# Kernel tuning notes

Measured on AMD Instinct MI355X. Metric: run time of the kernel, lower is better.

The kernel has to match this reference:

```python
import jax, jax.numpy as jnp
import numpy as np

H = 8; DH = 32; MAX_HOP = 256; NUM_EDGE = 25
NHOP = MAX_HOP + 2   # 258 (incl. UNREACHABLE)
NEDGE = NUM_EDGE + 2 # 27  (incl. NO_EDGE)


def _ln(x, g, b, eps=1e-5):
    m = x.mean(-1, keepdims=True)
    v = ((x - m) ** 2).mean(-1, keepdims=True)
    return (x - m) / jnp.sqrt(v + eps) * g + b


def _scatter_bins(att, idx, M):
    # att: [B,H,N,N] probs, idx: [B,N,N] int bins -> [B,H,N,M] scatter-add over keys
    B, Hh, N, _ = att.shape
    idxb = jnp.broadcast_to(idx[:, None, :, :], att.shape)
    bi = jnp.arange(B)[:, None, None, None]
    hi = jnp.arange(Hh)[None, :, None, None]
    ni = jnp.arange(N)[None, None, :, None]
    return jnp.zeros((B, Hh, N, M), att.dtype).at[bi, hi, ni, idxb].add(att)


def _forward(x, mask, distance_mat, edge_attr_mat,
             node_W, node_b, ln1_g, ln1_b, Wq, bq, Wk, bk, Wv, bv, Wo, bo,
             ln2_g, ln2_b, W1, b1, W2, b2,
             q_hop, q_edge, k_hop, k_edge, v_hop, v_edge,
             fln_g, fln_b, out_W, out_b):
    B, N, _ = x.shape
    h = x @ node_W + node_b  # [B,N,DM]
    # index preprocessing (clamp then -1 -> sentinel, as in torch)
    dist = jnp.minimum(distance_mat, MAX_HOP)
    dist = jnp.where(dist == -1, MAX_HOP + 1, dist)
    edge = jnp.minimum(edge_attr_mat, NUM_EDGE)
    edge = jnp.where(edge == -1, NUM_EDGE + 1, edge)

    # ---- encoder layer ----
    y = _ln(h, ln1_g, ln1_b)
    q = (y @ Wq + bq).reshape(B, N, H, DH).transpose(0, 2, 1, 3)  # bhnd
    k = (y @ Wk + bk).reshape(B, N, H, DH).transpose(0, 2, 1, 3)
    v = (y @ Wv + bv).reshape(B, N, H, DH).transpose(0, 2, 1, 3)
    Qh = q_hop.reshape(NHOP, H, DH).transpose(1, 0, 2)   # [H,M,d]
    Qe = q_edge.reshape(NEDGE, H, DH).transpose(1, 0, 2)
    Kh = k_hop.reshape(NHOP, H, DH).transpose(1, 0, 2)
    Ke = k_edge.reshape(NEDGE, H, DH).transpose(1, 0, 2)
    Vh = v_hop.reshape(NHOP, H, DH).transpose(1, 0, 2)
    Ve = v_edge.reshape(NEDGE, H, DH).transpose(1, 0, 2)

    dist_b = jnp.broadcast_to(dist[:, None, :, :], (B, H, N, N))
    edge_b = jnp.broadcast_to(edge[:, None, :, :], (B, H, N, N))

    qh = jnp.einsum('bhnd,hmd->bhnm', q, Qh)  # [B,H,N,M]
    query_hop = jnp.take_along_axis(qh, dist_b, axis=3)
    qe = jnp.einsum('bhnd,hmd->bhnm', q, Qe)
    query_edge = jnp.take_along_axis(qe, edge_b, axis=3)
    kh = jnp.einsum('bhnd,hmd->bhnm', k, Kh)
    # torch gathers along dim 2 of kh^T: key_hop[b,h,i,j] = k_j . Kh[dist[i,j]]
    key_hop = jnp.take_along_axis(jnp.swapaxes(kh, 2, 3), dist_b, axis=2)
    ke = jnp.einsum('bhnd,hmd->bhnm', k, Ke)
    key_edge = jnp.take_along_axis(ke, edge_b, axis=3)

    scale = DH ** (-0.5)
    scores = (jnp.einsum('bhid,bhjd->bhij', q, k)
              + (query_hop + key_hop) + (query_edge + key_edge)) * scale
    scores = jnp.where(mask[:, None, None, :], -jnp.inf, scores)
    att = jax.nn.softmax(scores, axis=-1)

    vha = _scatter_bins(att, dist, NHOP)   # [B,H,N,NHOP]
    vea = _scatter_bins(att, edge, NEDGE)
    ctx = (jnp.einsum('bhij,bhjd->bhid', att, v)
           + jnp.einsum('bhim,hmd->bhid', vha, Vh)
           + jnp.einsum('bhim,hmd->bhid', vea, Ve))
    ctx = ctx.transpose(0, 2, 1, 3).reshape(B, N, H * DH)
    h = h + (ctx @ Wo + bo)

    y = _ln(h, ln2_g, ln2_b)
    y = jax.nn.gelu(y @ W1 + b1, approximate=False) @ W2 + b2
    h = h + y
    # ---- head ----
    out = _ln(h, fln_g, fln_b)
    return out @ out_W + out_b


def setup_inputs() -> dict:
    key = jax.random.key(0)
    ks = jax.random.split(key, 40)
    D_IN, DM, FF, OUT, B, N = 128, 256, 1024, 128, 16, 512
    nrm = lambda k, shape, s=0.02: jax.random.normal(k, shape, jnp.float32) * s
    z = lambda shape: jnp.zeros(shape, jnp.float32)
    o = lambda shape: jnp.ones(shape, jnp.float32)
    return {
        'x': jax.random.normal(ks[0], (B, N, D_IN), jnp.float32),
        'mask': jnp.zeros((B, N), bool),
        'distance_mat': jax.random.randint(ks[1], (B, N, N), 0, 257),
        'edge_attr_mat': jax.random.randint(ks[2], (B, N, N), 0, 26),
        'node_W': nrm(ks[3], (D_IN, DM)), 'node_b': z((DM,)),
        'ln1_g': o((DM,)), 'ln1_b': z((DM,)),
        'Wq': nrm(ks[4], (DM, DM)), 'bq': z((DM,)),
        'Wk': nrm(ks[5], (DM, DM)), 'bk': z((DM,)),
        'Wv': nrm(ks[6], (DM, DM)), 'bv': z((DM,)),
        'Wo': nrm(ks[7], (DM, DM)), 'bo': z((DM,)),
        'ln2_g': o((DM,)), 'ln2_b': z((DM,)),
        'W1': nrm(ks[8], (DM, FF)), 'b1': z((FF,)),
        'W2': nrm(ks[9], (FF, DM)), 'b2': z((DM,)),
        'q_hop': nrm(ks[10], (NHOP, DM)), 'q_edge': nrm(ks[11], (NEDGE, DM)),
        'k_hop': nrm(ks[12], (NHOP, DM)), 'k_edge': nrm(ks[13], (NEDGE, DM)),
        'v_hop': nrm(ks[14], (NHOP, DM)), 'v_edge': nrm(ks[15], (NEDGE, DM)),
        'fln_g': o((DM,)), 'fln_b': z((DM,)),
        'out_W': nrm(ks[16], (DM, OUT)), 'out_b': z((OUT,)),
    }


def reference(x, mask, distance_mat, edge_attr_mat,
              node_W, node_b, ln1_g, ln1_b, Wq, bq, Wk, bk, Wv, bv, Wo, bo,
              ln2_g, ln2_b, W1, b1, W2, b2,
              q_hop, q_edge, k_hop, k_edge, v_hop, v_edge,
              fln_g, fln_b, out_W, out_b):
    return _forward(x, mask, distance_mat, edge_attr_mat,
                    node_W, node_b, ln1_g, ln1_b, Wq, bq, Wk, bk, Wv, bv, Wo, bo,
                    ln2_g, ln2_b, W1, b1, W2, b2,
                    q_hop, q_edge, k_hop, k_edge, v_hop, v_edge,
                    fln_g, fln_b, out_W, out_b)
```

## Files before the change

kernel.cpp:

```cpp
#include <hip/hip_runtime.h>
#include <hip/hip_bf16.h>
#include <math.h>

#define BB 16
#define NN 512
#define DIN 128
#define DM 256
#define NH 8
#define DH 32
#define FF 1024
#define DOUT 128
#define NHOP 258
#define NEDGE 27
#define ROWS (BB*NN)
#define QHE_S 296

typedef short short8 __attribute__((ext_vector_type(8)));
typedef float f32x4 __attribute__((ext_vector_type(4)));

static __device__ __forceinline__ float bf2f(unsigned short u) {
    union { float f; unsigned int i; } c; c.i = ((unsigned int)u) << 16; return c.f;
}
static __device__ __forceinline__ short f2bs(float f) {
    __hip_bfloat16 h = __float2bfloat16(f);
    return *reinterpret_cast<short*>(&h);
}

__global__ __launch_bounds__(256) void k_ln(const float* __restrict__ in, const float* __restrict__ g,
                                            const float* __restrict__ bta, float* __restrict__ out) {
    int row = blockIdx.x * 4 + (threadIdx.x >> 6);
    int l = threadIdx.x & 63;
    float4 xv = ((const float4*)(in + (size_t)row*DM))[l];
    float s = xv.x + xv.y + xv.z + xv.w;
    #pragma unroll
    for (int o = 32; o > 0; o >>= 1) s += __shfl_xor(s, o, 64);
    float mean = s * (1.0f/DM);
    float dx = xv.x-mean, dy = xv.y-mean, dz = xv.z-mean, dw = xv.w-mean;
    float vs = dx*dx + dy*dy + dz*dz + dw*dw;
    #pragma unroll
    for (int o = 32; o > 0; o >>= 1) vs += __shfl_xor(vs, o, 64);
    float r = rsqrtf(vs * (1.0f/DM) + 1e-5f);
    float4 gg = ((const float4*)g)[l];
    float4 bb = ((const float4*)bta)[l];
    float4 ov; ov.x = dx*r*gg.x+bb.x; ov.y = dy*r*gg.y+bb.y; ov.z = dz*r*gg.z+bb.z; ov.w = dw*r*gg.w+bb.w;
    ((float4*)(out + (size_t)row*DM))[l] = ov;
}

template<int K, int N, int ACT, int RES, int QKV>
__global__ __launch_bounds__(256) void k_mgemm(const float* __restrict__ A, const float* __restrict__ W,
                                               const float* __restrict__ bias, float* __restrict__ out) {
    __shared__ __align__(16) short As[64][40];
    __shared__ __align__(16) short Bs[64][40];
    int r0 = blockIdx.x * 64;
    int n0 = blockIdx.y * 64;
    int tid = threadIdx.x;
    int w = tid >> 6, l = tid & 63;

    f32x4 acc[4];
    #pragma unroll
    for (int c = 0; c < 4; ++c) acc[c] = (f32x4){0.f,0.f,0.f,0.f};

    for (int k0 = 0; k0 < K; k0 += 32) {
        __syncthreads();
        {
            int m = tid >> 2, ks = (tid & 3) * 8;
            const float* src = A + (size_t)(r0 + m)*K + k0 + ks;
            float4 f0 = *(const float4*)src;
            float4 f1 = *(const float4*)(src + 4);
            short8 pk;
            pk[0]=f2bs(f0.x); pk[1]=f2bs(f0.y); pk[2]=f2bs(f0.z); pk[3]=f2bs(f0.w);
            pk[4]=f2bs(f1.x); pk[5]=f2bs(f1.y); pk[6]=f2bs(f1.z); pk[7]=f2bs(f1.w);
            *(short8*)&As[m][ks] = pk;
        }
        {
            int n = tid & 63, kg = tid >> 6;
            const float* wp = W + (size_t)(k0 + kg*8)*N + n0 + n;
            short8 pk;
            #pragma unroll
            for (int j = 0; j < 8; ++j) pk[j] = f2bs(wp[(size_t)j*N]);
            *(short8*)&Bs[n][kg*8] = pk;
        }
        __syncthreads();
        short8 af = *(short8*)&As[w*16 + (l & 15)][(l >> 4)*8];
        #pragma unroll
        for (int c = 0; c < 4; ++c) {
            short8 bf = *(short8*)&Bs[c*16 + (l & 15)][(l >> 4)*8];
            acc[c] = __builtin_amdgcn_mfma_f32_16x16x32_bf16(af, bf, acc[c], 0, 0, 0);
        }
    }

    int quad = l >> 4;
    #pragma unroll
    for (int c = 0; c < 4; ++c) {
        int col = n0 + c*16 + (l & 15);
        float bv = bias[col];
        #pragma unroll
        for (int reg = 0; reg < 4; ++reg) {
            int row = r0 + w*16 + quad*4 + reg;
            float val = acc[c][reg] + bv;
            if (ACT) val = 0.5f * val * (1.0f + erff(val * 0.70710678118654752f));
            if (QKV) {
                int b = row >> 9, n = row & (NN-1);
                int hh = col >> 5, d = col & (DH-1);
                out[(size_t)((b*NH + hh)*NN + n)*DH + d] = val;
            } else if (RES) {
                out[(size_t)row*N + col] += val;
            } else {
                out[(size_t)row*N + col] = val;
            }
        }
    }
}

__global__ __launch_bounds__(256) void k_prep(const float* __restrict__ q_hop, const float* __restrict__ q_edge,
                                              const float* __restrict__ k_edge, const float* __restrict__ v_hop,
                                              const float* __restrict__ v_edge,
                                              unsigned short* __restrict__ w2, unsigned short* __restrict__ vhve_d) {
    int h = blockIdx.x;
    int tid = threadIdx.x;
    for (int idx = tid; idx < 304*64; idx += 256) {
        int n = idx >> 6, kk = idx & 63;
        float val = 0.f;
        if (n < NHOP && kk < 32) val = q_hop[(size_t)n*DM + h*DH + kk];
        else if (n >= 264 && n < 264 + NEDGE) {
            int e = n - 264;
            val = (kk < 32) ? q_edge[(size_t)e*DM + h*DH + kk]
                            : k_edge[(size_t)e*DM + h*DH + (kk - 32)];
        }
        w2[((size_t)h*304 + n)*64 + kk] = (unsigned short)f2bs(val);
    }
    for (int idx = tid; idx < 32*320; idx += 256) {
        int d = idx / 320, kk = idx - d*320;
        float val = 0.f;
        if (kk < NHOP) val = v_hop[(size_t)kk*DM + h*DH + d];
        else if (kk >= 264 && kk < 264 + NEDGE) val = v_edge[(size_t)(kk-264)*DM + h*DH + d];
        vhve_d[((size_t)h*32 + d)*320 + kk] = (unsigned short)f2bs(val);
    }
}

__global__ __launch_bounds__(256) void k_tx(const float* __restrict__ k, float* __restrict__ kT) {
    __shared__ float lds[64*33];
    int bh = blockIdx.x;
    int j0 = blockIdx.y * 64;
    int tid = threadIdx.x;
    {
        int jj = tid >> 2, d8 = tid & 3;
        const float* src = k + ((size_t)bh*NN + j0 + jj)*DH + d8*8;
        float4 a = *(const float4*)(src);
        float4 b = *(const float4*)(src + 4);
        float* dst = lds + jj*33 + d8*8;
        dst[0]=a.x; dst[1]=a.y; dst[2]=a.z; dst[3]=a.w;
        dst[4]=b.x; dst[5]=b.y; dst[6]=b.z; dst[7]=b.w;
    }
    __syncthreads();
    {
        int d = tid >> 3, jg = tid & 7;
        float* dst = kT + ((size_t)bh*DH + d)*NN + j0;
        #pragma unroll
        for (int jj2 = 0; jj2 < 8; ++jj2) {
            int j = jg*8 + jj2;
            dst[j] = lds[j*33 + d];
        }
    }
}

__global__ __launch_bounds__(256) void k_kht2(const float* __restrict__ k, const float* __restrict__ k_hop,
                                              __hip_bfloat16* __restrict__ kht) {
    __shared__ __align__(16) short kb[512][40];
    int bh = blockIdx.x;
    int hh = bh & (NH-1);
    int r0 = blockIdx.y * 64;
    int tid = threadIdx.x;
    int w = tid >> 6, l = tid & 63;
    int quad = l >> 4, lr = l & 15;

    #pragma unroll
    for (int t = 0; t < 8; ++t) {
        int idx = tid + t*256;
        int row = idx >> 2, c = idx & 3;
        const float* src = k + ((size_t)bh*NN + row)*DH + c*8;
        float4 f0 = *(const float4*)src;
        float4 f1 = *(const float4*)(src + 4);
        short8 pk;
        pk[0]=f2bs(f0.x); pk[1]=f2bs(f0.y); pk[2]=f2bs(f0.z); pk[3]=f2bs(f0.w);
        pk[4]=f2bs(f1.x); pk[5]=f2bs(f1.y); pk[6]=f2bs(f1.z); pk[7]=f2bs(f1.w);
        *(short8*)&kb[row][c*8] = pk;
    }
    int m = r0 + w*16 + lr;
    int mc = m < NHOP ? m : NHOP-1;
    const float* ar = k_hop + (size_t)mc*DM + hh*DH + quad*8;
    float4 a0 = *(const float4*)ar;
    float4 a1 = *(const float4*)(ar + 4);
    short8 af;
    af[0]=f2bs(a0.x); af[1]=f2bs(a0.y); af[2]=f2bs(a0.z); af[3]=f2bs(a0.w);
    af[4]=f2bs(a1.x); af[5]=f2bs(a1.y); af[6]=f2bs(a1.z); af[7]=f2bs(a1.w);
    __syncthreads();

    for (int ct = 0; ct < 32; ++ct) {
        short8 bf = *(short8*)&kb[ct*16 + lr][quad*8];
        f32x4 acc = (f32x4){0.f,0.f,0.f,0.f};
        acc = __builtin_amdgcn_mfma_f32_16x16x32_bf16(af, bf, acc, 0, 0, 0);
        #pragma unroll
        for (int reg = 0; reg < 4; ++reg) {
            int m2 = r0 + w*16 + quad*4 + reg;
            if (m2 < NHOP)
                kht[((size_t)bh*NHOP + m2)*NN + ct*16 + lr] = __float2bfloat16(acc[reg]);
        }
    }
}

__global__ __launch_bounds__(256) void k_qhe2(const float* __restrict__ q, const float* __restrict__ k,
                                              const unsigned short* __restrict__ w2,
                                              unsigned short* __restrict__ qhe) {
    int bh = blockIdx.x;
    int hh = bh & (NH-1);
    int r0 = blockIdx.y * 64;
    int tid = threadIdx.x;
    int w = tid >> 6, l = tid & 63;
    int quad = l >> 4, lr = l & 15;

    const float* qr = q + ((size_t)bh*NN + r0 + w*16 + lr)*DH + quad*8;
    const float* kr = k + ((size_t)bh*NN + r0 + w*16 + lr)*DH + quad*8;
    float4 f0 = *(const float4*)qr, f1 = *(const float4*)(qr + 4);
    short8 af0;
    af0[0]=f2bs(f0.x); af0[1]=f2bs(f0.y); af0[2]=f2bs(f0.z); af0[3]=f2bs(f0.w);
    af0[4]=f2bs(f1.x); af0[5]=f2bs(f1.y); af0[6]=f2bs(f1.z); af0[7]=f2bs(f1.w);
    f0 = *(const float4*)kr; f1 = *(const float4*)(kr + 4);
    short8 af1;
    af1[0]=f2bs(f0.x); af1[1]=f2bs(f0.y); af1[2]=f2bs(f0.z); af1[3]=f2bs(f0.w);
    af1[4]=f2bs(f1.x); af1[5]=f2bs(f1.y); af1[6]=f2bs(f1.z); af1[7]=f2bs(f1.w);

    const unsigned short* w2h = w2 + (size_t)hh*304*64;
    for (int ct = 0; ct < 19; ++ct) {
        int col = ct*16 + lr;
        short8 b0 = *(const short8*)(w2h + (size_t)col*64 + quad*8);
        short8 b1 = *(const short8*)(w2h + (size_t)col*64 + 32 + quad*8);
        f32x4 acc = (f32x4){0.f,0.f,0.f,0.f};
        acc = __builtin_amdgcn_mfma_f32_16x16x32_bf16(af0, b0, acc, 0, 0, 0);
        acc = __builtin_amdgcn_mfma_f32_16x16x32_bf16(af1, b1, acc, 0, 0, 0);
        if (col < QHE_S) {
            #pragma unroll
            for (int reg = 0; reg < 4; ++reg) {
                int row = r0 + w*16 + quad*4 + reg;
                qhe[((size_t)bh*NN + row)*QHE_S + col] = (unsigned short)f2bs(acc[reg]);
            }
        }
    }
}

__global__ __launch_bounds__(256) void k_score(
    const float* __restrict__ q, const float* __restrict__ kT, const float* __restrict__ v,
    const __hip_bfloat16* __restrict__ kht, const int* __restrict__ dist, const int* __restrict__ edge,
    const unsigned char* __restrict__ mask, unsigned short* __restrict__ qhe,
    float* __restrict__ ctx)
{
    int g   = blockIdx.x;
    int r   = g >> 3;
    int b   = (g & 7) + ((r >> 8) << 3);
    int rem = r & 255;
    int i0  = (rem >> 1) * 4;
    int hg  = rem & 1;
    int w   = threadIdx.x >> 6;
    int l   = threadIdx.x & 63;
    int hh  = hg*4 + w;
    int bh  = b*NH + hh;

    __shared__ unsigned short mje[4][NN];
    __shared__ float qv[4][4][DH];
    __shared__ __hip_bfloat16 pb[4][4][NN];
    __shared__ float bins[4][292];

    {
        int t = threadIdx.x;
        int row = t >> 6, c0 = t & 63;
        #pragma unroll
        for (int rep = 0; rep < 2; ++rep) {
            int c4 = c0 + rep*64;
            int4 dv = ((const int4*)(dist + ((size_t)(b*NN) + i0 + row)*NN))[c4];
            int4 ev = ((const int4*)(edge + ((size_t)(b*NN) + i0 + row)*NN))[c4];
            int m0 = dv.x > 256 ? 256 : dv.x; if (dv.x < 0) m0 = 257;
            int m1 = dv.y > 256 ? 256 : dv.y; if (dv.y < 0) m1 = 257;
            int m2 = dv.z > 256 ? 256 : dv.z; if (dv.z < 0) m2 = 257;
            int m3 = dv.w > 256 ? 256 : dv.w; if (dv.w < 0) m3 = 257;
            int e0 = ev.x > 25 ? 25 : ev.x; if (ev.x < 0) e0 = 26;
            int e1 = ev.y > 25 ? 25 : ev.y; if (ev.y < 0) e1 = 26;
            int e2 = ev.z > 25 ? 25 : ev.z; if (ev.z < 0) e2 = 26;
            int e3 = ev.w > 25 ? 25 : ev.w; if (ev.w < 0) e3 = 26;
            mje[row][c4*4+0] = (unsigned short)(m0 | (e0 << 9));
            mje[row][c4*4+1] = (unsigned short)(m1 | (e1 << 9));
            mje[row][c4*4+2] = (unsigned short)(m2 | (e2 << 9));
            mje[row][c4*4+3] = (unsigned short)(m3 | (e3 << 9));
        }
        #pragma unroll
        for (int rep = 0; rep < 2; ++rep) {
            int i = rep*2 + (l >> 5), d = l & 31;
            qv[w][i][d] = q[((size_t)bh*NN + i0 + i)*DH + d];
        }
        for (int s = l; s < 292; s += 64) bins[w][s] = 0.f;
    }
    __syncthreads();

    float sc[4][8];
    #pragma unroll
    for (int i = 0; i < 4; ++i)
        #pragma unroll
        for (int s = 0; s < 8; ++s) sc[i][s] = 0.f;
    {
        const float* kTb = kT + (size_t)bh*DH*NN;
        for (int d = 0; d < 32; ++d) {
            const float* kr = kTb + (size_t)d*NN + l;
            float k0 = kr[0],   k1 = kr[64],  k2 = kr[128], k3 = kr[192];
            float k4 = kr[256], k5 = kr[320], k6 = kr[384], k7 = kr[448];
            float qa = qv[w][0][d], qb = qv[w][1][d], qc = qv[w][2][d], qd = qv[w][3][d];
            sc[0][0]+=qa*k0; sc[0][1]+=qa*k1; sc[0][2]+=qa*k2; sc[0][3]+=qa*k3;
            sc[0][4]+=qa*k4; sc[0][5]+=qa*k5; sc[0][6]+=qa*k6; sc[0][7]+=qa*k7;
            sc[1][0]+=qb*k0; sc[1][1]+=qb*k1; sc[1][2]+=qb*k2; sc[1][3]+=qb*k3;
            sc[1][4]+=qb*k4; sc[1][5]+=qb*k5; sc[1][6]+=qb*k6; sc[1][7]+=qb*k7;
            sc[2][0]+=qc*k0; sc[2][1]+=qc*k1; sc[2][2]+=qc*k2; sc[2][3]+=qc*k3;
            sc[2][4]+=qc*k4; sc[2][5]+=qc*k5; sc[2][6]+=qc*k6; sc[2][7]+=qc*k7;
            sc[3][0]+=qd*k0; sc[3][1]+=qd*k1; sc[3][2]+=qd*k2; sc[3][3]+=qd*k3;
            sc[3][4]+=qd*k4; sc[3][5]+=qd*k5; sc[3][6]+=qd*k6; sc[3][7]+=qd*k7;
        }
    }

    const __hip_bfloat16* khtb = kht + (size_t)bh*NHOP*NN;
    const unsigned char* mrow = mask + (size_t)b*NN;
    unsigned char msk[8];
    #pragma unroll
    for (int s = 0; s < 8; ++s) msk[s] = mrow[l + 64*s];
    const float scale = 0.17677669529663687f;

    #pragma unroll
    for (int i = 0; i < 4; ++i) {
        unsigned short* qhr = qhe + ((size_t)bh*NN + i0 + i)*QHE_S;
        int pk[8];
        #pragma unroll
        for (int s = 0; s < 8; ++s) pk[s] = mje[i][l + 64*s];
        unsigned short raw[8];
        #pragma unroll
        for (int s = 0; s < 8; ++s)
            raw[s] = ((const unsigned short*)khtb)[(size_t)(pk[s] & 511)*NN + l + 64*s];
        unsigned short qhv[8], qev[8];
        #pragma unroll
        for (int s = 0; s < 8; ++s) qhv[s] = qhr[pk[s] & 511];
        #pragma unroll
        for (int s = 0; s < 8; ++s) qev[s] = qhr[264 + (pk[s] >> 9)];
        float x[8];
        #pragma unroll
        for (int s = 0; s < 8; ++s) {
            float a = (sc[i][s] + bf2f(qhv[s]) + bf2f(raw[s]) + bf2f(qev[s])) * scale;
            if (msk[s]) a = -INFINITY;
            x[s] = a;
        }
        float mx = x[0];
        #pragma unroll
        for (int s = 1; s < 8; ++s) mx = fmaxf(mx, x[s]);
        #pragma unroll
        for (int o = 32; o > 0; o >>= 1) mx = fmaxf(mx, __shfl_xor(mx, o, 64));
        float sum = 0.f;
        #pragma unroll
        for (int s = 0; s < 8; ++s) { x[s] = __expf(x[s] - mx); sum += x[s]; }
        #pragma unroll
        for (int o = 32; o > 0; o >>= 1) sum += __shfl_xor(sum, o, 64);
        float inv = 1.0f / sum;
        #pragma unroll
        for (int s = 0; s < 8; ++s) {
            float ps = x[s] * inv;
            pb[w][i][l + 64*s] = __float2bfloat16(ps);
            atomicAdd(&bins[w][pk[s] & 511], ps);
            atomicAdd(&bins[w][264 + (pk[s] >> 9)], ps);
        }
        #pragma unroll
        for (int s5 = 0; s5 < 5; ++s5) {
            int idx = l + 64*s5;
            if (idx < 292) {
                qhr[idx] = (unsigned short)f2bs(bins[w][idx]);
                if (i < 3) bins[w][idx] = 0.f;
            }
        }
    }

    int jc = l >> 3, d4 = l & 7;
    float4 acc[4];
    #pragma unroll
    for (int i = 0; i < 4; ++i) { acc[i].x = acc[i].y = acc[i].z = acc[i].w = 0.f; }
    {
        const float* vb = v + (size_t)bh*NN*DH + d4*4;
        for (int off = 0; off < 64; ++off) {
            int j = 8*off + jc;
            float4 vv = *(const float4*)(vb + (size_t)j*DH);
            #pragma unroll
            for (int i = 0; i < 4; ++i) {
                float p = bf2f(*(const unsigned short*)&pb[w][i][j]);
                acc[i].x += p*vv.x; acc[i].y += p*vv.y; acc[i].z += p*vv.z; acc[i].w += p*vv.w;
            }
        }
    }
    #pragma unroll
    for (int i = 0; i < 4; ++i) {
        #pragma unroll
        for (int o = 8; o <= 32; o <<= 1) {
            acc[i].x += __shfl_xor(acc[i].x, o, 64);
            acc[i].y += __shfl_xor(acc[i].y, o, 64);
            acc[i].z += __shfl_xor(acc[i].z, o, 64);
            acc[i].w += __shfl_xor(acc[i].w, o, 64);
        }
        if (jc == 0) {
            *(float4*)(ctx + ((size_t)b*NN + i0 + i)*DM + hh*DH + d4*4) = acc[i];
        }
    }
}

__global__ __launch_bounds__(256) void k_av2(const unsigned short* __restrict__ vha,
                                             const unsigned short* __restrict__ vhve_d,
                                             float* __restrict__ ctx) {
    int bh = blockIdx.x;
    int hh = bh & (NH-1);
    int b  = bh >> 3;
    int r0 = blockIdx.y * 64;
    int tid = threadIdx.x;
    int w = tid >> 6, l = tid & 63;
    int quad = l >> 4, lr = l & 15;

    const unsigned short* arow = vha + ((size_t)bh*NN + r0 + w*16 + lr)*QHE_S + quad*8;
    const unsigned short* br0  = vhve_d + ((size_t)hh*32 + lr)*320 + quad*8;
    const unsigned short* br1  = vhve_d + ((size_t)hh*32 + 16 + lr)*320 + quad*8;

    f32x4 acc0 = (f32x4){0.f,0.f,0.f,0.f};
    f32x4 acc1 = (f32x4){0.f,0.f,0.f,0.f};
    #pragma unroll
    for (int k0 = 0; k0 < 320; k0 += 32) {
        short8 af = *(const short8*)(arow + k0);
        short8 b0 = *(const short8*)(br0 + k0);
        short8 b1 = *(const short8*)(br1 + k0);
        acc0 = __builtin_amdgcn_mfma_f32_16x16x32_bf16(af, b0, acc0, 0, 0, 0);
        acc1 = __builtin_amdgcn_mfma_f32_16x16x32_bf16(af, b1, acc1, 0, 0, 0);
    }
    #pragma unroll
    for (int reg = 0; reg < 4; ++reg) {
        int row = r0 + w*16 + quad*4 + reg;
        float* cp = ctx + ((size_t)b*NN + row)*DM + hh*DH;
        cp[lr]      += acc0[reg];
        cp[16 + lr] += acc1[reg];
    }
}

extern "C" void kernel_launch(void* const* d_in, const int* in_sizes, int n_in,
                              void* d_out, int out_size, void* d_ws, size_t ws_size,
                              hipStream_t stream) {
    const float* x     = (const float*)d_in[0];
    const unsigned char* mask = (const unsigned char*)d_in[1];
    const int*   dist  = (const int*)d_in[2];
    const int*   edge  = (const int*)d_in[3];
    const float* node_W = (const float*)d_in[4];
    const float* node_b = (const float*)d_in[5];
    const float* ln1_g = (const float*)d_in[6];
    const float* ln1_b = (const float*)d_in[7];
    const float* Wq = (const float*)d_in[8];
    const float* bq = (const float*)d_in[9];
    const float* Wk = (const float*)d_in[10];
    const float* bk = (const float*)d_in[11];
    const float* Wv = (const float*)d_in[12];
    const float* bv = (const float*)d_in[13];
    const float* Wo = (const float*)d_in[14];
    const float* bo = (const float*)d_in[15];
    const float* ln2_g = (const float*)d_in[16];
    const float* ln2_b = (const float*)d_in[17];
    const float* W1 = (const float*)d_in[18];
    const float* b1 = (const float*)d_in[19];
    const float* W2 = (const float*)d_in[20];
    const float* b2 = (const float*)d_in[21];
    const float* q_hop  = (const float*)d_in[22];
    const float* q_edge = (const float*)d_in[23];
    const float* k_hop  = (const float*)d_in[24];
    const float* k_edge = (const float*)d_in[25];
    const float* v_hop  = (const float*)d_in[26];
    const float* v_edge = (const float*)d_in[27];
    const float* fln_g = (const float*)d_in[28];
    const float* fln_b = (const float*)d_in[29];
    const float* out_W = (const float*)d_in[30];
    const float* out_b = (const float*)d_in[31];
    float* out = (float*)d_out;

    float* ws = (float*)d_ws;
    float* h   = ws + 0;
    float* y   = ws + 2097152;
    float* q   = ws + 4194304;
    float* k   = ws + 6291456;
    float* v   = ws + 8388608;
    float* ctx = ws + 10485760;
    __hip_bfloat16* kht = (__hip_bfloat16*)(ws + 12582912);
    float* ffn = ws + 12582912;
    float* kT  = ws + 21037056;
    unsigned short* qhe = (unsigned short*)(ws + 23134208);
    unsigned short* w2     = (unsigned short*)(y);
    unsigned short* vhve_d = (unsigned short*)(y + 81920);

    k_mgemm<DIN, DM, 0, 0, 0><<<dim3(ROWS/64, DM/64), 256, 0, stream>>>(x, node_W, node_b, h);
    k_ln<<<ROWS/4, 256, 0, stream>>>(h, ln1_g, ln1_b, y);
    k_mgemm<DM, DM, 0, 0, 1><<<dim3(ROWS/64, DM/64), 256, 0, stream>>>(y, Wq, bq, q);
    k_mgemm<DM, DM, 0, 0, 1><<<dim3(ROWS/64, DM/64), 256, 0, stream>>>(y, Wk, bk, k);
    k_mgemm<DM, DM, 0, 0, 1><<<dim3(ROWS/64, DM/64), 256, 0, stream>>>(y, Wv, bv, v);
    k_prep<<<NH, 256, 0, stream>>>(q_hop, q_edge, k_edge, v_hop, v_edge, w2, vhve_d);
    k_tx<<<dim3(BB*NH, 8), 256, 0, stream>>>(k, kT);
    k_kht2<<<dim3(BB*NH, 5), 256, 0, stream>>>(k, k_hop, kht);
    k_qhe2<<<dim3(BB*NH, NN/64), 256, 0, stream>>>(q, k, w2, qhe);
    k_score<<<BB*(NN/4)*2, 256, 0, stream>>>(q, kT, v, kht, dist, edge, mask, qhe, ctx);
    k_av2<<<dim3(BB*NH, NN/64), 256, 0, stream>>>(qhe, vhve_d, ctx);
    k_mgemm<DM, DM, 0, 1, 0><<<dim3(ROWS/64, DM/64), 256, 0, stream>>>(ctx, Wo, bo, h);
    k_ln<<<ROWS/4, 256, 0, stream>>>(h, ln2_g, ln2_b, y);
    k_mgemm<DM, FF, 1, 0, 0><<<dim3(ROWS/64, FF/64), 256, 0, stream>>>(y, W1, b1, ffn);
    k_mgemm<FF, DM, 0, 1, 0><<<dim3(ROWS/64, DM/64), 256, 0, stream>>>(ffn, W2, b2, h);
    k_ln<<<ROWS/4, 256, 0, stream>>>(h, fln_g, fln_b, y);
    k_mgemm<DM, DOUT, 0, 0, 0><<<dim3(ROWS/64, DOUT/64), 256, 0, stream>>>(y, out_W, out_b, out);
}
```

Measured before the change: 739.5 us.

## Emit bf16 Q/K/V^T from projections and use MFMA for attention scores and PV

The Q/K/V projection GEMMs now write bf16 outputs, with V written pre-transposed, so the separate K transpose kernel and the per-kernel fp32-to-bf16 conversions go away. The score kernel is restructured so each block handles 16 query rows of one head. QK^T and P·V are computed with bf16 MFMA instructions instead of scalar FMA loops, and the softmax is reduced across waves through shared memory. This aims to cut FP32 ALU work and memory traffic, at the cost of more shared memory per block, extra block-level syncs, and bf16 rounding of q, k and v.

Measured after the change: 719.7 us. 2.7% less time.

```diff
diff --git a/kernel.cpp b/kernel.cpp
--- a/kernel.cpp
+++ b/kernel.cpp
@@ -48,7 +48,7 @@
 
 template<int K, int N, int ACT, int RES, int QKV>
 __global__ __launch_bounds__(256) void k_mgemm(const float* __restrict__ A, const float* __restrict__ W,
-                                               const float* __restrict__ bias, float* __restrict__ out) {
+                                               const float* __restrict__ bias, void* __restrict__ outv) {
     __shared__ __align__(16) short As[64][40];
     __shared__ __align__(16) short Bs[64][40];
     int r0 = blockIdx.x * 64;
@@ -99,14 +99,20 @@
             int row = r0 + w*16 + quad*4 + reg;
             float val = acc[c][reg] + bv;
             if (ACT) val = 0.5f * val * (1.0f + erff(val * 0.70710678118654752f));
-            if (QKV) {
+            if (QKV == 1) {
+                unsigned short* out = (unsigned short*)outv;
                 int b = row >> 9, n = row & (NN-1);
                 int hh = col >> 5, d = col & (DH-1);
-                out[(size_t)((b*NH + hh)*NN + n)*DH + d] = val;
+                out[(size_t)((b*NH + hh)*NN + n)*DH + d] = (unsigned short)f2bs(val);
+            } else if (QKV == 2) {
+                unsigned short* out = (unsigned short*)outv;
+                int b = row >> 9, n = row & (NN-1);
+                int hh = col >> 5, d = col & (DH-1);
+                out[(size_t)((b*NH + hh)*DH + d)*NN + n] = (unsigned short)f2bs(val);
             } else if (RES) {
-                out[(size_t)row*N + col] += val;
+                ((float*)outv)[(size_t)row*N + col] += val;
             } else {
-                out[(size_t)row*N + col] = val;
+                ((float*)outv)[(size_t)row*N + col] = val;
             }
         }
     }
@@ -138,35 +144,9 @@
     }
 }
 
-__global__ __launch_bounds__(256) void k_tx(const float* __restrict__ k, float* __restrict__ kT) {
-    __shared__ float lds[64*33];
-    int bh = blockIdx.x;
-    int j0 = blockIdx.y * 64;
-    int tid = threadIdx.x;
-    {
-        int jj = tid >> 2, d8 = tid & 3;
-        const float* src = k + ((size_t)bh*NN + j0 + jj)*DH + d8*8;
-        float4 a = *(const float4*)(src);
-        float4 b = *(const float4*)(src + 4);
-        float* dst = lds + jj*33 + d8*8;
-        dst[0]=a.x; dst[1]=a.y; dst[2]=a.z; dst[3]=a.w;
-        dst[4]=b.x; dst[5]=b.y; dst[6]=b.z; dst[7]=b.w;
-    }
-    __syncthreads();
-    {
-        int d = tid >> 3, jg = tid & 7;
-        float* dst = kT + ((size_t)bh*DH + d)*NN + j0;
-        #pragma unroll
-        for (int jj2 = 0; jj2 < 8; ++jj2) {
-            int j = jg*8 + jj2;
-            dst[j] = lds[j*33 + d];
-        }
-    }
-}
-
-__global__ __launch_bounds__(256) void k_kht2(const float* __restrict__ k, const float* __restrict__ k_hop,
-                                              __hip_bfloat16* __restrict__ kht) {
-    __shared__ __align__(16) short kb[512][40];
+__global__ __launch_bounds__(256) void k_kht2(const unsigned short* __restrict__ k_bf,
+                                              const float* __restrict__ k_hop,
+                                              unsigned short* __restrict__ kht) {
     int bh = blockIdx.x;
     int hh = bh & (NH-1);
     int r0 = blockIdx.y * 64;
@@ -174,18 +154,6 @@
     int w = tid >> 6, l = tid & 63;
     int quad = l >> 4, lr = l & 15;
 
-    #pragma unroll
-    for (int t = 0; t < 8; ++t) {
-        int idx = tid + t*256;
-        int row = idx >> 2, c = idx & 3;
-        const float* src = k + ((size_t)bh*NN + row)*DH + c*8;
-        float4 f0 = *(const float4*)src;
-        float4 f1 = *(const float4*)(src + 4);
-        short8 pk;
-        pk[0]=f2bs(f0.x); pk[1]=f2bs(f0.y); pk[2]=f2bs(f0.z); pk[3]=f2bs(f0.w);
-        pk[4]=f2bs(f1.x); pk[5]=f2bs(f1.y); pk[6]=f2bs(f1.z); pk[7]=f2bs(f1.w);
-        *(short8*)&kb[row][c*8] = pk;
-    }
     int m = r0 + w*16 + lr;
     int mc = m < NHOP ? m : NHOP-1;
     const float* ar = k_hop + (size_t)mc*DM + hh*DH + quad*8;
@@ -194,22 +162,22 @@
     short8 af;
     af[0]=f2bs(a0.x); af[1]=f2bs(a0.y); af[2]=f2bs(a0.z); af[3]=f2bs(a0.w);
     af[4]=f2bs(a1.x); af[5]=f2bs(a1.y); af[6]=f2bs(a1.z); af[7]=f2bs(a1.w);
-    __syncthreads();
 
     for (int ct = 0; ct < 32; ++ct) {
-        short8 bf = *(short8*)&kb[ct*16 + lr][quad*8];
+        short8 bf = *(const short8*)(k_bf + ((size_t)bh*NN + ct*16 + lr)*DH + quad*8);
         f32x4 acc = (f32x4){0.f,0.f,0.f,0.f};
         acc = __builtin_amdgcn_mfma_f32_16x16x32_bf16(af, bf, acc, 0, 0, 0);
         #pragma unroll
         for (int reg = 0; reg < 4; ++reg) {
             int m2 = r0 + w*16 + quad*4 + reg;
             if (m2 < NHOP)
-                kht[((size_t)bh*NHOP + m2)*NN + ct*16 + lr] = __float2bfloat16(acc[reg]);
-        }
-    }
-}
-
-__global__ __launch_bounds__(256) void k_qhe2(const float* __restrict__ q, const float* __restrict__ k,
+                kht[((size_t)bh*NHOP + m2)*NN + ct*16 + lr] = (unsigned short)f2bs(acc[reg]);
+        }
+    }
+}
+
+__global__ __launch_bounds__(256) void k_qhe2(const unsigned short* __restrict__ q_bf,
+                                              const unsigned short* __restrict__ k_bf,
                                               const unsigned short* __restrict__ w2,
                                               unsigned short* __restrict__ qhe) {
     int bh = blockIdx.x;
@@ -219,16 +187,9 @@
     int w = tid >> 6, l = tid & 63;
     int quad = l >> 4, lr = l & 15;
 
-    const float* qr = q + ((size_t)bh*NN + r0 + w*16 + lr)*DH + quad*8;
-    const float* kr = k + ((size_t)bh*NN + r0 + w*16 + lr)*DH + quad*8;
-    float4 f0 = *(const float4*)qr, f1 = *(const float4*)(qr + 4);
-    short8 af0;
-    af0[0]=f2bs(f0.x); af0[1]=f2bs(f0.y); af0[2]=f2bs(f0.z); af0[3]=f2bs(f0.w);
-    af0[4]=f2bs(f1.x); af0[5]=f2bs(f1.y); af0[6]=f2bs(f1.z); af0[7]=f2bs(f1.w);
-    f0 = *(const float4*)kr; f1 = *(const float4*)(kr + 4);
-    short8 af1;
-    af1[0]=f2bs(f0.x); af1[1]=f2bs(f0.y); af1[2]=f2bs(f0.z); af1[3]=f2bs(f0.w);
-    af1[4]=f2bs(f1.x); af1[5]=f2bs(f1.y); af1[6]=f2bs(f1.z); af1[7]=f2bs(f1.w);
+    int row0 = r0 + w*16 + lr;
+    short8 af0 = *(const short8*)(q_bf + ((size_t)bh*NN + row0)*DH + quad*8);
+    short8 af1 = *(const short8*)(k_bf + ((size_t)bh*NN + row0)*DH + quad*8);
 
     const unsigned short* w2h = w2 + (size_t)hh*304*64;
     for (int ct = 0; ct < 19; ++ct) {
@@ -249,35 +210,36 @@
 }
 
 __global__ __launch_bounds__(256) void k_score(
-    const float* __restrict__ q, const float* __restrict__ kT, const float* __restrict__ v,
-    const __hip_bfloat16* __restrict__ kht, const int* __restrict__ dist, const int* __restrict__ edge,
+    const unsigned short* __restrict__ q_bf, const unsigned short* __restrict__ k_bf,
+    const unsigned short* __restrict__ vT_bf, const unsigned short* __restrict__ kht,
+    const int* __restrict__ dist, const int* __restrict__ edge,
     const unsigned char* __restrict__ mask, unsigned short* __restrict__ qhe,
     float* __restrict__ ctx)
 {
-    int g   = blockIdx.x;
-    int r   = g >> 3;
-    int b   = (g & 7) + ((r >> 8) << 3);
+    int g = blockIdx.x;
+    int r = g >> 3;
+    int b = (g & 7) + ((r >> 8) << 3);
     int rem = r & 255;
-    int i0  = (rem >> 1) * 4;
-    int hg  = rem & 1;
-    int w   = threadIdx.x >> 6;
-    int l   = threadIdx.x & 63;
-    int hh  = hg*4 + w;
-    int bh  = b*NH + hh;
-
-    __shared__ unsigned short mje[4][NN];
-    __shared__ float qv[4][4][DH];
-    __shared__ __hip_bfloat16 pb[4][4][NN];
-    __shared__ float bins[4][292];
+    int hh = rem >> 5;
+    int i0 = (rem & 31) << 4;
+    int bh = b*NH + hh;
+    int tid = threadIdx.x;
+    int w = tid >> 6, l = tid & 63;
+    int lr = l & 15, quad = l >> 4;
+
+    __shared__ __align__(16) unsigned short mje[16][512];
+    __shared__ __align__(16) unsigned short Pl[16][520];
+    __shared__ float bins[16][292];
+    __shared__ float red[2][4][16];
+    float* cpart = (float*)&mje[0][0];
 
     {
-        int t = threadIdx.x;
-        int row = t >> 6, c0 = t & 63;
-        #pragma unroll
-        for (int rep = 0; rep < 2; ++rep) {
-            int c4 = c0 + rep*64;
-            int4 dv = ((const int4*)(dist + ((size_t)(b*NN) + i0 + row)*NN))[c4];
-            int4 ev = ((const int4*)(edge + ((size_t)(b*NN) + i0 + row)*NN))[c4];
+        const int4* dp = (const int4*)(dist + ((size_t)b*NN + i0)*NN);
+        const int4* ep = (const int4*)(edge + ((size_t)b*NN + i0)*NN);
+        unsigned short* mf = &mje[0][0];
+        for (int idx = tid; idx < 2048; idx += 256) {
+            int4 dv = dp[idx];
+            int4 ev = ep[idx];
             int m0 = dv.x > 256 ? 256 : dv.x; if (dv.x < 0) m0 = 257;
             int m1 = dv.y > 256 ? 256 : dv.y; if (dv.y < 0) m1 = 257;
             int m2 = dv.z > 256 ? 256 : dv.z; if (dv.z < 0) m2 = 257;
@@ -286,128 +248,138 @@
             int e1 = ev.y > 25 ? 25 : ev.y; if (ev.y < 0) e1 = 26;
             int e2 = ev.z > 25 ? 25 : ev.z; if (ev.z < 0) e2 = 26;
             int e3 = ev.w > 25 ? 25 : ev.w; if (ev.w < 0) e3 = 26;
-            mje[row][c4*4+0] = (unsigned short)(m0 | (e0 << 9));
-            mje[row][c4*4+1] = (unsigned short)(m1 | (e1 << 9));
-            mje[row][c4*4+2] = (unsigned short)(m2 | (e2 << 9));
-            mje[row][c4*4+3] = (unsigned short)(m3 | (e3 << 9));
-        }
-        #pragma unroll
-        for (int rep = 0; rep < 2; ++rep) {
-            int i = rep*2 + (l >> 5), d = l & 31;
-            qv[w][i][d] = q[((size_t)bh*NN + i0 + i)*DH + d];
-        }
-        for (int s = l; s < 292; s += 64) bins[w][s] = 0.f;
+            uint2 pk;
+            pk.x = (unsigned)(m0 | (e0<<9)) | ((unsigned)(m1 | (e1<<9)) << 16);
+            pk.y = (unsigned)(m2 | (e2<<9)) | ((unsigned)(m3 | (e3<<9)) << 16);
+            *(uint2*)&mf[idx*4] = pk;
+        }
+        float* bf_ = &bins[0][0];
+        for (int idx = tid; idx < 16*292; idx += 256) bf_[idx] = 0.f;
     }
     __syncthreads();
 
-    float sc[4][8];
-    #pragma unroll
-    for (int i = 0; i < 4; ++i)
-        #pragma unroll
-        for (int s = 0; s < 8; ++s) sc[i][s] = 0.f;
+    int jbase = w*128;
+    short8 af = *(const short8*)(q_bf + ((size_t)bh*NN + i0 + lr)*DH + quad*8);
+    f32x4 sc[8];
+    #pragma unroll
+    for (int ct = 0; ct < 8; ++ct) {
+        short8 bfr = *(const short8*)(k_bf + ((size_t)bh*NN + jbase + ct*16 + lr)*DH + quad*8);
+        f32x4 z = (f32x4){0.f,0.f,0.f,0.f};
+        sc[ct] = __builtin_amdgcn_mfma_f32_16x16x32_bf16(af, bfr, z, 0, 0, 0);
+    }
+
+    const unsigned short* khtb = kht + (size_t)bh*NHOP*NN;
+    const unsigned char* mrow = mask + (size_t)b*NN;
+    const float scale = 0.17677669529663687f;
+    unsigned char msk[8];
+    #pragma unroll
+    for (int ct = 0; ct < 8; ++ct) msk[ct] = mrow[jbase + ct*16 + lr];
+
+    #pragma unroll
+    for (int ct = 0; ct < 8; ++ct) {
+        int j = jbase + ct*16 + lr;
+        #pragma unroll
+        for (int reg = 0; reg < 4; ++reg) {
+            int il = quad*4 + reg;
+            int pk = mje[il][j];
+            int m = pk & 511, e = pk >> 9;
+            const unsigned short* qhr = qhe + ((size_t)bh*NN + i0 + il)*QHE_S;
+            float a = sc[ct][reg] + bf2f(khtb[(size_t)m*NN + j]) + bf2f(qhr[m]) + bf2f(qhr[264 + e]);
+            a *= scale;
+            if (msk[ct]) a = -INFINITY;
+            sc[ct][reg] = a;
+        }
+    }
+
     {
-        const float* kTb = kT + (size_t)bh*DH*NN;
-        for (int d = 0; d < 32; ++d) {
-            const float* kr = kTb + (size_t)d*NN + l;
-            float k0 = kr[0],   k1 = kr[64],  k2 = kr[128], k3 = kr[192];
-            float k4 = kr[256], k5 = kr[320], k6 = kr[384], k7 = kr[448];
-            float qa = qv[w][0][d], qb = qv[w][1][d], qc = qv[w][2][d], qd = qv[w][3][d];
-            sc[0][0]+=qa*k0; sc[0][1]+=qa*k1; sc[0][2]+=qa*k2; sc[0][3]+=qa*k3;
-            sc[0][4]+=qa*k4; sc[0][5]+=qa*k5; sc[0][6]+=qa*k6; sc[0][7]+=qa*k7;
-            sc[1][0]+=qb*k0; sc[1][1]+=qb*k1; sc[1][2]+=qb*k2; sc[1][3]+=qb*k3;
-            sc[1][4]+=qb*k4; sc[1][5]+=qb*k5; sc[1][6]+=qb*k6; sc[1][7]+=qb*k7;
-            sc[2][0]+=qc*k0; sc[2][1]+=qc*k1; sc[2][2]+=qc*k2; sc[2][3]+=qc*k3;
-            sc[2][4]+=qc*k4; sc[2][5]+=qc*k5; sc[2][6]+=qc*k6; sc[2][7]+=qc*k7;
-            sc[3][0]+=qd*k0; sc[3][1]+=qd*k1; sc[3][2]+=qd*k2; sc[3][3]+=qd*k3;
-            sc[3][4]+=qd*k4; sc[3][5]+=qd*k5; sc[3][6]+=qd*k6; sc[3][7]+=qd*k7;
-        }
-    }
-
-    const __hip_bfloat16* khtb = kht + (size_t)bh*NHOP*NN;
-    const unsigned char* mrow = mask + (size_t)b*NN;
-    unsigned char msk[8];
-    #pragma unroll
-    for (int s = 0; s < 8; ++s) msk[s] = mrow[l + 64*s];
-    const float scale = 0.17677669529663687f;
-
-    #pragma unroll
-    for (int i = 0; i < 4; ++i) {
-        unsigned short* qhr = qhe + ((size_t)bh*NN + i0 + i)*QHE_S;
-        int pk[8];
-        #pragma unroll
-        for (int s = 0; s < 8; ++s) pk[s] = mje[i][l + 64*s];
-        unsigned short raw[8];
-        #pragma unroll
-        for (int s = 0; s < 8; ++s)
-            raw[s] = ((const unsigned short*)khtb)[(size_t)(pk[s] & 511)*NN + l + 64*s];
-        unsigned short qhv[8], qev[8];
-        #pragma unroll
-        for (int s = 0; s < 8; ++s) qhv[s] = qhr[pk[s] & 511];
-        #pragma unroll
-        for (int s = 0; s < 8; ++s) qev[s] = qhr[264 + (pk[s] >> 9)];
-        float x[8];
-        #pragma unroll
-        for (int s = 0; s < 8; ++s) {
-            float a = (sc[i][s] + bf2f(qhv[s]) + bf2f(raw[s]) + bf2f(qev[s])) * scale;
-            if (msk[s]) a = -INFINITY;
-            x[s] = a;
-        }
-        float mx = x[0];
-        #pragma unroll
-        for (int s = 1; s < 8; ++s) mx = fmaxf(mx, x[s]);
-        #pragma unroll
-        for (int o = 32; o > 0; o >>= 1) mx = fmaxf(mx, __shfl_xor(mx, o, 64));
-        float sum = 0.f;
-        #pragma unroll
-        for (int s = 0; s < 8; ++s) { x[s] = __expf(x[s] - mx); sum += x[s]; }
-        #pragma unroll
-        for (int o = 32; o > 0; o >>= 1) sum += __shfl_xor(sum, o, 64);
-        float inv = 1.0f / sum;
-        #pragma unroll
-        for (int s = 0; s < 8; ++s) {
-            float ps = x[s] * inv;
-            pb[w][i][l + 64*s] = __float2bfloat16(ps);
-            atomicAdd(&bins[w][pk[s] & 511], ps);
-            atomicAdd(&bins[w][264 + (pk[s] >> 9)], ps);
-        }
-        #pragma unroll
-        for (int s5 = 0; s5 < 5; ++s5) {
-            int idx = l + 64*s5;
-            if (idx < 292) {
-                qhr[idx] = (unsigned short)f2bs(bins[w][idx]);
-                if (i < 3) bins[w][idx] = 0.f;
+        float mymax[4];
+        #pragma unroll
+        for (int reg = 0; reg < 4; ++reg) {
+            float mx = sc[0][reg];
+            #pragma unroll
+            for (int ct = 1; ct < 8; ++ct) mx = fmaxf(mx, sc[ct][reg]);
+            #pragma unroll
+            for (int o = 1; o < 16; o <<= 1) mx = fmaxf(mx, __shfl_xor(mx, o, 16));
+            mymax[reg] = mx;
+        }
+        if (lr == 0) {
+            #pragma unroll
+            for (int reg = 0; reg < 4; ++reg) red[0][w][quad*4 + reg] = mymax[reg];
+        }
+        __syncthreads();
+        float mysum[4];
+        #pragma unroll
+        for (int reg = 0; reg < 4; ++reg) {
+            int il = quad*4 + reg;
+            float mx = fmaxf(fmaxf(red[0][0][il], red[0][1][il]), fmaxf(red[0][2][il], red[0][3][il]));
+            float s = 0.f;
+            #pragma unroll
+            for (int ct = 0; ct < 8; ++ct) { float ex = __expf(sc[ct][reg] - mx); sc[ct][reg] = ex; s += ex; }
+            #pragma unroll
+            for (int o = 1; o < 16; o <<= 1) s += __shfl_xor(s, o, 16);
+            mysum[reg] = s;
+        }
+        if (lr == 0) {
+            #pragma unroll
+            for (int reg = 0; reg < 4; ++reg) red[1][w][quad*4 + reg] = mysum[reg];
+        }
+        __syncthreads();
+        float inv_[4];
+        #pragma unroll
+        for (int reg = 0; reg < 4; ++reg) {
+            int il = quad*4 + reg;
+            inv_[reg] = 1.0f / (red[1][0][il] + red[1][1][il] + red[1][2][il] + red[1][3][il]);
+        }
+        #pragma unroll
+        for (int ct = 0; ct < 8; ++ct) {
+            int j = jbase + ct*16 + lr;
+            #pragma unroll
+            for (int reg = 0; reg < 4; ++reg) {
+                int il = quad*4 + reg;
+                float ps = sc[ct][reg] * inv_[reg];
+                Pl[il][j] = (unsigned short)f2bs(ps);
+                int pk = mje[il][j];
+                atomicAdd(&bins[il][pk & 511], ps);
+                atomicAdd(&bins[il][264 + (pk >> 9)], ps);
             }
         }
     }
-
-    int jc = l >> 3, d4 = l & 7;
-    float4 acc[4];
-    #pragma unroll
-    for (int i = 0; i < 4; ++i) { acc[i].x = acc[i].y = acc[i].z = acc[i].w = 0.f; }
+    __syncthreads();
+
     {
-        const float* vb = v + (size_t)bh*NN*DH + d4*4;
-        for (int off = 0; off < 64; ++off) {
-            int j = 8*off + jc;
-            float4 vv = *(const float4*)(vb + (size_t)j*DH);
-            #pragma unroll
-            for (int i = 0; i < 4; ++i) {
-                float p = bf2f(*(const unsigned short*)&pb[w][i][j]);
-                acc[i].x += p*vv.x; acc[i].y += p*vv.y; acc[i].z += p*vv.z; acc[i].w += p*vv.w;
-            }
-        }
-    }
-    #pragma unroll
-    for (int i = 0; i < 4; ++i) {
-        #pragma unroll
-        for (int o = 8; o <= 32; o <<= 1) {
-            acc[i].x += __shfl_xor(acc[i].x, o, 64);
-            acc[i].y += __shfl_xor(acc[i].y, o, 64);
-            acc[i].z += __shfl_xor(acc[i].z, o, 64);
-            acc[i].w += __shfl_xor(acc[i].w, o, 64);
-        }
-        if (jc == 0) {
-            *(float4*)(ctx + ((size_t)b*NN + i0 + i)*DM + hh*DH + d4*4) = acc[i];
-        }
+        int rowd = tid >> 4, c0 = tid & 15;
+        unsigned short* dst = qhe + ((size_t)bh*NN + i0 + rowd)*QHE_S;
+        for (int c = c0; c < 292; c += 16) dst[c] = (unsigned short)f2bs(bins[rowd][c]);
+    }
+
+    f32x4 acc0 = (f32x4){0.f,0.f,0.f,0.f};
+    f32x4 acc1 = (f32x4){0.f,0.f,0.f,0.f};
+    #pragma unroll
+    for (int t = 0; t < 4; ++t) {
+        int kk = jbase + t*32 + quad*8;
+        short8 pa = *(const short8*)&Pl[lr][kk];
+        short8 b0 = *(const short8*)(vT_bf + ((size_t)bh*DH + lr)*NN + kk);
+        short8 b1 = *(const short8*)(vT_bf + ((size_t)bh*DH + 16 + lr)*NN + kk);
+        acc0 = __builtin_amdgcn_mfma_f32_16x16x32_bf16(pa, b0, acc0, 0, 0, 0);
+        acc1 = __builtin_amdgcn_mfma_f32_16x16x32_bf16(pa, b1, acc1, 0, 0, 0);
+    }
+    #pragma unroll
+    for (int reg = 0; reg < 4; ++reg) {
+        int il = quad*4 + reg;
+        cpart[((size_t)w*16 + il)*32 + lr]      = acc0[reg];
+        cpart[((size_t)w*16 + il)*32 + 16 + lr] = acc1[reg];
+    }
+    __syncthreads();
+    {
+        int rowd = tid >> 4, dd = (tid & 15)*2;
+        float v0 = 0.f, v1 = 0.f;
+        #pragma unroll
+        for (int ww = 0; ww < 4; ++ww) {
+            v0 += cpart[((size_t)ww*16 + rowd)*32 + dd];
+            v1 += cpart[((size_t)ww*16 + rowd)*32 + dd + 1];
+        }
+        float* cp = ctx + ((size_t)b*NN + i0 + rowd)*DM + hh*DH + dd;
+        cp[0] = v0; cp[1] = v1;
     }
 }
 
@@ -485,27 +457,25 @@
     float* ws = (float*)d_ws;
     float* h   = ws + 0;
     float* y   = ws + 2097152;
-    float* q   = ws + 4194304;
-    float* k   = ws + 6291456;
-    float* v   = ws + 8388608;
-    float* ctx = ws + 10485760;
-    __hip_bfloat16* kht = (__hip_bfloat16*)(ws + 12582912);
-    float* ffn = ws + 12582912;
-    float* kT  = ws + 21037056;
-    unsigned short* qhe = (unsigned short*)(ws + 23134208);
+    unsigned short* q_bf  = (unsigned short*)(ws + 4194304);
+    unsigned short* k_bf  = (unsigned short*)(ws + 5242880);
+    unsigned short* vT_bf = (unsigned short*)(ws + 6291456);
+    float* ctx = ws + 7340032;
+    unsigned short* kht = (unsigned short*)(ws + 9437184);
+    float* ffn = ws + 9437184;
+    unsigned short* qhe = (unsigned short*)(ws + 17891328);
     unsigned short* w2     = (unsigned short*)(y);
     unsigned short* vhve_d = (unsigned short*)(y + 81920);
 
     k_mgemm<DIN, DM, 0, 0, 0><<<dim3(ROWS/64, DM/64), 256, 0, stream>>>(x, node_W, node_b, h);
     k_ln<<<ROWS/4, 256, 0, stream>>>(h, ln1_g, ln1_b, y);
-    k_mgemm<DM, DM, 0, 0, 1><<<dim3(ROWS/64, DM/64), 256, 0, stream>>>(y, Wq, bq, q);
-    k_mgemm<DM, DM, 0, 0, 1><<<dim3(ROWS/64, DM/64), 256, 0, stream>>>(y, Wk, bk, k);
-    k_mgemm<DM, DM, 0, 0, 1><<<dim3(ROWS/64, DM/64), 256, 0, stream>>>(y, Wv, bv, v);
+    k_mgemm<DM, DM, 0, 0, 1><<<dim3(ROWS/64, DM/64), 256, 0, stream>>>(y, Wq, bq, q_bf);
+    k_mgemm<DM, DM, 0, 0, 1><<<dim3(ROWS/64, DM/64), 256, 0, stream>>>(y, Wk, bk, k_bf);
+    k_mgemm<DM, DM, 0, 0, 2><<<dim3(ROWS/64, DM/64), 256, 0, stream>>>(y, Wv, bv, vT_bf);
     k_prep<<<NH, 256, 0, stream>>>(q_hop, q_edge, k_edge, v_hop, v_edge, w2, vhve_d);
-    k_tx<<<dim3(BB*NH, 8), 256, 0, stream>>>(k, kT);
-    k_kht2<<<dim3(BB*NH, 5), 256, 0, stream>>>(k, k_hop, kht);
-    k_qhe2<<<dim3(BB*NH, NN/64), 256, 0, stream>>>(q, k, w2, qhe);
-    k_score<<<BB*(NN/4)*2, 256, 0, stream>>>(q, kT, v, kht, dist, edge, mask, qhe, ctx);
+    k_kht2<<<dim3(BB*NH, 5), 256, 0, stream>>>(k_bf, k_hop, kht);
+    k_qhe2<<<dim3(BB*NH, NN/64), 256, 0, stream>>>(q_bf, k_bf, w2, qhe);
+    k_score<<<BB*NH*(NN/16), 256, 0, stream>>>(q_bf, k_bf, vT_bf, kht, dist, edge, mask, qhe, ctx);
     k_av2<<<dim3(BB*NH, NN/64), 256, 0, stream>>>(qhe, vhve_d, ctx);
     k_mgemm<DM, DM, 0, 1, 0><<<dim3(ROWS/64, DM/64), 256, 0, stream>>>(ctx, Wo, bo, h);
     k_ln<<<ROWS/4, 256, 0, stream>>>(h, ln2_g, ln2_b, y);
```
